# Performance work log

Measured on AMD Instinct MI355X. Metric: run time of the kernel, lower is better.

The kernel has to match this reference:

```python
import jax, jax.numpy as jnp
import numpy as np

N, E, D, H, O = 100000, 1600000, 256, 128, 64


def setup_inputs() -> dict:
    key = jax.random.key(0)
    ks = jax.random.split(key, 10)
    x = jax.random.normal(ks[0], (N, D), dtype=jnp.float32)
    # edges without self loops (original adds remaining self loops itself)
    row = jax.random.randint(ks[1], (E,), 0, N)
    off = jax.random.randint(ks[2], (E,), 1, N)
    col = (row + off) % N
    edge_index = jnp.stack([row, col]).astype(jnp.int64)
    # positive PPMI edge weights (stand-in for cached random-walk PPMI values)
    ppmi_edge_weight = jax.random.uniform(ks[3], (E,), dtype=jnp.float32, minval=0.1, maxval=1.0)
    # glorot-style weights (shared between GCN and PPMI branches, as in the module)
    W1 = jax.random.normal(ks[4], (D, H), dtype=jnp.float32) * np.sqrt(2.0 / (D + H))
    b1 = jnp.zeros((H,), dtype=jnp.float32)
    W2 = jax.random.normal(ks[5], (H, O), dtype=jnp.float32) * np.sqrt(2.0 / (H + O))
    b2 = jnp.zeros((O,), dtype=jnp.float32)
    dense_w = jax.random.normal(ks[6], (O, 1), dtype=jnp.float32) * np.sqrt(2.0 / (O + 1))
    dense_b = jnp.zeros((1,), dtype=jnp.float32)
    return {"x": x, "edge_index": edge_index, "ppmi_edge_weight": ppmi_edge_weight,
            "W1": W1, "b1": b1, "W2": W2, "b2": b2,
            "dense_w": dense_w, "dense_b": dense_b}


def _sym_norm(row, col, ew, n):
    # deg^-0.5[row] * w * deg^-0.5[col], deg from scatter-add over source index
    deg = jax.ops.segment_sum(ew, row, num_segments=n)
    dis = jnp.where(deg > 0, deg ** -0.5, 0.0)
    return dis[row] * ew * dis[col]


def _gconv(h, W, b, row, col, norm, n):
    hw = h @ W                              # [N, F_out]
    msg = norm[:, None] * hw[row]           # gather + scale, [E', F_out]
    return jax.ops.segment_sum(msg, col, num_segments=n) + b


def reference(x, edge_index, ppmi_edge_weight, W1, b1, W2, b2, dense_w, dense_b):
    n = x.shape[0]
    row = edge_index[0].astype(jnp.int32)
    col = edge_index[1].astype(jnp.int32)
    sl = jnp.arange(n, dtype=jnp.int32)
    row_sl = jnp.concatenate([row, sl])
    col_sl = jnp.concatenate([col, sl])
    ones_sl = jnp.ones((n,), dtype=x.dtype)

    # GCN branch: edge_weight = 1, plus self loops (fill_value = 1)
    gcn_ew = jnp.concatenate([jnp.ones((row.shape[0],), dtype=x.dtype), ones_sl])
    gnorm = _sym_norm(row_sl, col_sl, gcn_ew, n)
    g = jax.nn.relu(_gconv(x, W1, b1, row_sl, col_sl, gnorm, n))  # dropout p in eval -> identity
    g = _gconv(g, W2, b2, row_sl, col_sl, gnorm, n)

    # PPMI branch: precomputed positive weights, plus self loops
    ppmi_ew = jnp.concatenate([ppmi_edge_weight.astype(x.dtype), ones_sl])
    pnorm = _sym_norm(row_sl, col_sl, ppmi_ew, n)
    p = jax.nn.relu(_gconv(x, W1, b1, row_sl, col_sl, pnorm, n))
    p = _gconv(p, W2, b2, row_sl, col_sl, pnorm, n)

    stacked = jnp.stack([g, p], axis=1)                 # [N, 2, O]
    logits = stacked @ dense_w + dense_b                # [N, 2, 1]
    w = jax.nn.softmax(logits, axis=1)
    return jnp.sum(stacked * w, axis=1)                 # [N, O]
```

## Files before the change

kernel.cpp:

```cpp
#include <hip/hip_runtime.h>
#include <hip/hip_bf16.h>
#include <math.h>

#define DD 256
#define HH 128
#define OO 64

#define EPB 8192
#define BKT 512

typedef __attribute__((ext_vector_type(8))) __bf16 bf16x8;
typedef __attribute__((ext_vector_type(4))) __bf16 bf16x4;
typedef __attribute__((ext_vector_type(4))) float f32x4;

__device__ inline float2 bf2_to_f2(unsigned u) {
    float2 r;
    r.x = __uint_as_float(u << 16);
    r.y = __uint_as_float(u & 0xffff0000u);
    return r;
}

__global__ void part_count_kernel(const int* __restrict__ row, const int* __restrict__ col,
                                  int e, int nb,
                                  int* __restrict__ cnt_col, int* __restrict__ cnt_row) {
    __shared__ int hc[256], hr[256];
    int t = threadIdx.x;
    hc[t] = 0; hr[t] = 0;
    __syncthreads();
    int base = blockIdx.x * EPB;
    int lim  = min(EPB, e - base);
    for (int i = t; i < lim; i += 256) {
        atomicAdd(&hc[col[base + i] >> 9], 1);
        atomicAdd(&hr[row[base + i] >> 9], 1);
    }
    __syncthreads();
    if (t < nb) {
        cnt_col[blockIdx.x * nb + t] = hc[t];
        cnt_row[blockIdx.x * nb + t] = hr[t];
    }
}

__global__ void scan_blocks_kernel(const int* __restrict__ cnt_col, const int* __restrict__ cnt_row,
                                   int* __restrict__ base_col, int* __restrict__ base_row,
                                   int* __restrict__ tot_col, int* __restrict__ tot_row,
                                   int nblk, int nb) {
    __shared__ int s[256];
    int side = (blockIdx.x >= (unsigned)nb) ? 1 : 0;
    int b = blockIdx.x - side * nb;
    const int* cnt = side ? cnt_row : cnt_col;
    int* base = side ? base_row : base_col;
    int* tot  = side ? tot_row  : tot_col;
    int t = threadIdx.x;
    int v = (t < nblk) ? cnt[(size_t)t * nb + b] : 0;
    s[t] = v;
    __syncthreads();
    for (int off = 1; off < 256; off <<= 1) {
        int u = (t >= off) ? s[t - off] : 0;
        __syncthreads();
        s[t] += u;
        __syncthreads();
    }
    if (t < nblk) base[(size_t)t * nb + b] = s[t] - v;
    if (t == 255) tot[b] = s[255];
}

__global__ void scan_tots_kernel(const int* __restrict__ tot_col, const int* __restrict__ tot_row,
                                 int* __restrict__ bb_col, int* __restrict__ bb_row, int nb) {
    __shared__ int s[256];
    int t = threadIdx.x;
    int v = (t < nb) ? tot_col[t] : 0;
    s[t] = v;
    __syncthreads();
    for (int off = 1; off < 256; off <<= 1) {
        int u = (t >= off) ? s[t - off] : 0;
        __syncthreads();
        s[t] += u;
        __syncthreads();
    }
    if (t < nb) bb_col[t] = s[t] - v;
    __syncthreads();
    int v2 = (t < nb) ? tot_row[t] : 0;
    s[t] = v2;
    __syncthreads();
    for (int off = 1; off < 256; off <<= 1) {
        int u = (t >= off) ? s[t - off] : 0;
        __syncthreads();
        s[t] += u;
        __syncthreads();
    }
    if (t < nb) bb_row[t] = s[t] - v2;
}

__global__ void add_bases_kernel(int* __restrict__ base_col, int* __restrict__ base_row,
                                 const int* __restrict__ bb_col, const int* __restrict__ bb_row,
                                 int* __restrict__ row_ptr, int n, int e, int nblk, int nb) {
    int side = (blockIdx.x >= (unsigned)nb) ? 1 : 0;
    int b = blockIdx.x - side * nb;
    int* base = side ? base_row : base_col;
    int add   = side ? bb_row[b] : bb_col[b];
    for (int t = threadIdx.x; t < nblk; t += blockDim.x) base[(size_t)t * nb + b] += add;
    if (blockIdx.x == 0 && threadIdx.x == 0) row_ptr[n] = e;
}

__global__ void part_scatter_kernel(const int* __restrict__ row, const int* __restrict__ col,
                                    const float* __restrict__ ppmi,
                                    const int* __restrict__ base_col, const int* __restrict__ base_row,
                                    int4* __restrict__ tmp_col, int2* __restrict__ tmp_row,
                                    int e, int nb) {
    __shared__ int cc[256], cr[256];
    int t = threadIdx.x;
    if (t < nb) {
        cc[t] = base_col[blockIdx.x * nb + t];
        cr[t] = base_row[blockIdx.x * nb + t];
    }
    __syncthreads();
    int base = blockIdx.x * EPB;
    int lim  = min(EPB, e - base);
    for (int i = t; i < lim; i += 256) {
        int r = row[base + i], c = col[base + i];
        int w = __float_as_int(ppmi[base + i]);
        int sc = atomicAdd(&cc[c >> 9], 1);
        tmp_col[sc] = make_int4(c, r, w, 0);
        int sr = atomicAdd(&cr[r >> 9], 1);
        tmp_row[sr] = make_int2(r, w);
    }
}

__global__ void deg_bucket_kernel(const int2* __restrict__ tmp_row,
                                  const int* __restrict__ bb_row, const int* __restrict__ tot_row,
                                  float* __restrict__ dis_g, float* __restrict__ dis_p, int n) {
    __shared__ float dg[BKT], dp[BKT];
    int t = threadIdx.x;
    for (int j = t; j < BKT; j += 256) { dg[j] = 1.0f; dp[j] = 1.0f; }
    __syncthreads();
    int b = blockIdx.x;
    int beg = bb_row[b], cnt = tot_row[b];
    for (int i = t; i < cnt; i += 256) {
        int2 cell = tmp_row[beg + i];
        int lr = cell.x & (BKT - 1);
        atomicAdd(&dg[lr], 1.0f);
        atomicAdd(&dp[lr], __int_as_float(cell.y));
    }
    __syncthreads();
    int rb = b << 9;
    for (int j = t; j < BKT; j += 256) {
        int g = rb + j;
        if (g < n) {
            dis_g[g] = rsqrtf(dg[j]);
            dis_p[g] = rsqrtf(dp[j]);
        }
    }
}

__launch_bounds__(512)
__global__ void csr_bucket_kernel(const int4* __restrict__ tmp_col,
                                  const int* __restrict__ bb_col, const int* __restrict__ tot_col,
                                  const float* __restrict__ dis_g, const float* __restrict__ dis_p,
                                  int* __restrict__ row_ptr, int* __restrict__ csr_src,
                                  float* __restrict__ csr_wg, float* __restrict__ csr_wp, int n) {
    __shared__ int hist[BKT], s[BKT], cur[BKT];
    int t = threadIdx.x;
    hist[t] = 0;
    __syncthreads();
    int b = blockIdx.x;
    int beg = bb_col[b], cnt = tot_col[b];
    for (int i = t; i < cnt; i += BKT) atomicAdd(&hist[tmp_col[beg + i].x & (BKT - 1)], 1);
    __syncthreads();
    int own = hist[t];
    s[t] = own;
    __syncthreads();
    for (int off = 1; off < BKT; off <<= 1) {
        int v = (t >= off) ? s[t - off] : 0;
        __syncthreads();
        s[t] += v;
        __syncthreads();
    }
    int gslot = beg + s[t] - own;
    cur[t] = gslot;
    int gc = (b << 9) + t;
    if (gc < n) row_ptr[gc] = gslot;
    __syncthreads();
    for (int i = t; i < cnt; i += BKT) {
        int4 cell = tmp_col[beg + i];
        int lc = cell.x & (BKT - 1);
        int slot = atomicAdd(&cur[lc], 1);
        int r = cell.y;
        float w = __int_as_float(cell.z);
        csr_src[slot] = r;
        csr_wg[slot]  = dis_g[r];
        csr_wp[slot]  = dis_p[r] * w;
    }
}

__global__ void conv_w_kernel(const float* __restrict__ W, __bf16* __restrict__ Bh,
                              __bf16* __restrict__ Bl, int K, int N) {
    int i = blockIdx.x * blockDim.x + threadIdx.x;
    if (i >= K * N) return;
    int k = i / N, nn = i % N;
    float v = W[i];
    __bf16 h = (__bf16)v;
    Bh[(size_t)nn * K + k] = h;
    Bl[(size_t)nn * K + k] = (__bf16)(v - (float)h);
}

template<int BM, int BN, typename OT>
__launch_bounds__(256, 2)
__global__ void mfma_gemm_kernel(const float* __restrict__ A,
                                 const __bf16* __restrict__ Bth, const __bf16* __restrict__ Btl,
                                 OT* __restrict__ C, int M, int K) {
    constexpr int BK  = 32;
    constexpr int LDK = BK + 8;
    constexpr int WM  = BM / 4;
    constexpr int MT  = WM / 16;
    constexpr int NT  = BN / 16;
    __shared__ __bf16 Ash[BM * LDK];
    __shared__ __bf16 Asl[BM * LDK];
    __shared__ __bf16 Bsh[BN * LDK];
    __shared__ __bf16 Bsl[BN * LDK];

    const int tid  = threadIdx.x;
    const int wave = tid >> 6;
    const int lane = tid & 63;
    const int quad = lane >> 4;
    const int l16  = lane & 15;
    const int row0 = blockIdx.x * BM;

    f32x4 acc[MT][NT] = {};

    for (int k0 = 0; k0 < K; k0 += BK) {
#pragma unroll
        for (int p = 0; p < BM / 32; ++p) {
            int lin = p * 256 + tid;
            int r   = lin >> 3;
            int kc  = (lin & 7) * 4;
            int gr  = row0 + r;
            float4 v;
            if (gr < M) v = *(const float4*)(A + (size_t)gr * K + k0 + kc);
            else        v = make_float4(0.f, 0.f, 0.f, 0.f);
            __bf16 h0 = (__bf16)v.x, h1 = (__bf16)v.y, h2 = (__bf16)v.z, h3 = (__bf16)v.w;
            __bf16 l0 = (__bf16)(v.x - (float)h0), l1 = (__bf16)(v.y - (float)h1);
            __bf16 l2 = (__bf16)(v.z - (float)h2), l3 = (__bf16)(v.w - (float)h3);
            *(bf16x4*)&Ash[r * LDK + kc] = (bf16x4){h0, h1, h2, h3};
            *(bf16x4*)&Asl[r * LDK + kc] = (bf16x4){l0, l1, l2, l3};
        }
#pragma unroll
        for (int p = 0; p < BN / 64; ++p) {
            int lin = p * 256 + tid;
            int r   = lin >> 2;
            int kc  = (lin & 3) * 8;
            *(uint4*)&Bsh[r * LDK + kc] = *(const uint4*)(Bth + (size_t)r * K + k0 + kc);
            *(uint4*)&Bsl[r * LDK + kc] = *(const uint4*)(Btl + (size_t)r * K + k0 + kc);
        }
        __syncthreads();

        bf16x8 bh[NT], bl[NT];
#pragma unroll
        for (int j = 0; j < NT; ++j) {
            bh[j] = *(const bf16x8*)&Bsh[(j * 16 + l16) * LDK + quad * 8];
            bl[j] = *(const bf16x8*)&Bsl[(j * 16 + l16) * LDK + quad * 8];
        }
#pragma unroll
        for (int i = 0; i < MT; ++i) {
            int m = wave * WM + i * 16 + l16;
            bf16x8 ah = *(const bf16x8*)&Ash[m * LDK + quad * 8];
            bf16x8 al = *(const bf16x8*)&Asl[m * LDK + quad * 8];
#pragma unroll
            for (int j = 0; j < NT; ++j) {
                acc[i][j] = __builtin_amdgcn_mfma_f32_16x16x32_bf16(ah, bh[j], acc[i][j], 0, 0, 0);
                acc[i][j] = __builtin_amdgcn_mfma_f32_16x16x32_bf16(ah, bl[j], acc[i][j], 0, 0, 0);
                acc[i][j] = __builtin_amdgcn_mfma_f32_16x16x32_bf16(al, bh[j], acc[i][j], 0, 0, 0);
            }
        }
        __syncthreads();
    }

#pragma unroll
    for (int i = 0; i < MT; ++i) {
#pragma unroll
        for (int rg = 0; rg < 4; ++rg) {
            int gr = row0 + wave * WM + i * 16 + quad * 4 + rg;
            if (gr < M) {
#pragma unroll
                for (int j = 0; j < NT; ++j)
                    C[(size_t)gr * BN + j * 16 + l16] = (OT)acc[i][j][rg];
            }
        }
    }
}

__global__ void agg1_pull_kernel(const int* __restrict__ row_ptr, const int* __restrict__ csr_src,
                                 const float* __restrict__ csr_wg, const float* __restrict__ csr_wp,
                                 const __bf16* __restrict__ hw1,
                                 const float* __restrict__ dis_g, const float* __restrict__ dis_p,
                                 const float* __restrict__ b1,
                                 float* __restrict__ g_out, float* __restrict__ p_out, int n) {
    int c    = blockIdx.x * 4 + (threadIdx.x >> 6);
    int lane = threadIdx.x & 63;
    if (c >= n) return;
    int beg = row_ptr[c], end = row_ptr[c + 1];
    int f2 = lane * 2;
    float sgx = 0.f, sgy = 0.f, spx = 0.f, spy = 0.f;
    int t = beg;
    for (; t + 2 <= end; t += 2) {
        int r0 = csr_src[t], r1 = csr_src[t + 1];
        float wg0 = csr_wg[t], wg1 = csr_wg[t + 1];
        float wp0 = csr_wp[t], wp1 = csr_wp[t + 1];
        float2 h0 = bf2_to_f2(*(const unsigned*)(hw1 + (size_t)r0 * HH + f2));
        float2 h1 = bf2_to_f2(*(const unsigned*)(hw1 + (size_t)r1 * HH + f2));
        sgx += wg0 * h0.x + wg1 * h1.x;
        sgy += wg0 * h0.y + wg1 * h1.y;
        spx += wp0 * h0.x + wp1 * h1.x;
        spy += wp0 * h0.y + wp1 * h1.y;
    }
    if (t < end) {
        int r0 = csr_src[t];
        float wg0 = csr_wg[t], wp0 = csr_wp[t];
        float2 h0 = bf2_to_f2(*(const unsigned*)(hw1 + (size_t)r0 * HH + f2));
        sgx += wg0 * h0.x; sgy += wg0 * h0.y;
        spx += wp0 * h0.x; spy += wp0 * h0.y;
    }
    float dgc = dis_g[c], dpc = dis_p[c];
    size_t idx = (size_t)c * HH + f2;
    float2 hs = bf2_to_f2(*(const unsigned*)(hw1 + idx));
    float bx = b1[f2], by = b1[f2 + 1];
    float gx = dgc * sgx + dgc * dgc * hs.x + bx;
    float gy = dgc * sgy + dgc * dgc * hs.y + by;
    float px = dpc * spx + dpc * dpc * hs.x + bx;
    float py = dpc * spy + dpc * dpc * hs.y + by;
    float2 go, po;
    go.x = gx > 0.f ? gx : 0.f;  go.y = gy > 0.f ? gy : 0.f;
    po.x = px > 0.f ? px : 0.f;  po.y = py > 0.f ? py : 0.f;
    *(float2*)&g_out[idx] = go;
    *(float2*)&p_out[idx] = po;
}

__global__ void agg2_final_kernel(const int* __restrict__ row_ptr, const int* __restrict__ csr_src,
                                  const float* __restrict__ csr_wg, const float* __restrict__ csr_wp,
                                  const __bf16* __restrict__ hw2_g, const __bf16* __restrict__ hw2_p,
                                  const float* __restrict__ dis_g, const float* __restrict__ dis_p,
                                  const float* __restrict__ b2,
                                  const float* __restrict__ dense_w, const float* __restrict__ dense_b,
                                  float* __restrict__ out, int n) {
    int c = blockIdx.x * 4 + (threadIdx.x >> 6);
    int f = threadIdx.x & 63;
    if (c >= n) return;
    int beg = row_ptr[c], end = row_ptr[c + 1];
    float sg = 0.f, sp = 0.f;
    int t = beg;
    for (; t + 2 <= end; t += 2) {
        int r0 = csr_src[t], r1 = csr_src[t + 1];
        float wg0 = csr_wg[t], wg1 = csr_wg[t + 1];
        float wp0 = csr_wp[t], wp1 = csr_wp[t + 1];
        float hg0 = (float)hw2_g[(size_t)r0 * OO + f], hg1 = (float)hw2_g[(size_t)r1 * OO + f];
        float hp0 = (float)hw2_p[(size_t)r0 * OO + f], hp1 = (float)hw2_p[(size_t)r1 * OO + f];
        sg += wg0 * hg0 + wg1 * hg1;
        sp += wp0 * hp0 + wp1 * hp1;
    }
    if (t < end) {
        int r0 = csr_src[t];
        sg += csr_wg[t] * (float)hw2_g[(size_t)r0 * OO + f];
        sp += csr_wp[t] * (float)hw2_p[(size_t)r0 * OO + f];
    }
    float dgc = dis_g[c], dpc = dis_p[c];
    size_t idx = (size_t)c * OO + f;
    float bb = b2[f];
    float gv = dgc * sg + dgc * dgc * (float)hw2_g[idx] + bb;
    float pv = dpc * sp + dpc * dpc * (float)hw2_p[idx] + bb;
    float dw = dense_w[f];
    float lg = gv * dw, lp = pv * dw;
#pragma unroll
    for (int off = 32; off > 0; off >>= 1) {
        lg += __shfl_xor(lg, off, 64);
        lp += __shfl_xor(lp, off, 64);
    }
    lg += dense_b[0];
    lp += dense_b[0];
    float m  = fmaxf(lg, lp);
    float eg = expf(lg - m), ep = expf(lp - m);
    float wgt = eg / (eg + ep);
    out[idx] = wgt * gv + (1.0f - wgt) * pv;
}

extern "C" void kernel_launch(void* const* d_in, const int* in_sizes, int n_in,
                              void* d_out, int out_size, void* d_ws, size_t ws_size,
                              hipStream_t stream) {
    const float* x    = (const float*)d_in[0];
    const int*   ei   = (const int*)d_in[1];
    const float* ppmi = (const float*)d_in[2];
    const float* W1   = (const float*)d_in[3];
    const float* b1   = (const float*)d_in[4];
    const float* W2   = (const float*)d_in[5];
    const float* b2   = (const float*)d_in[6];
    const float* dw   = (const float*)d_in[7];
    const float* db   = (const float*)d_in[8];
    float* out = (float*)d_out;

    const int n = in_sizes[0] / DD;
    const int e = in_sizes[2];
    const int* row = ei;
    const int* col = ei + e;

    const int nb   = (n + BKT - 1) / BKT;
    const int nblk = (e + EPB - 1) / EPB;

    float* ws     = (float*)d_ws;
    float* dis_g  = ws;
    float* dis_p  = dis_g + n;
    __bf16* hw1   = (__bf16*)(dis_p + n);
    float* g1     = (float*)(hw1 + (size_t)n * HH);
    float* p1     = g1  + (size_t)n * HH;
    float* csr_wg = p1  + (size_t)n * HH;
    float* csr_wp = csr_wg + e;
    __bf16* bt1h  = (__bf16*)(csr_wp + e);
    __bf16* bt1l  = bt1h + (size_t)DD * HH;
    __bf16* bt2h  = bt1l + (size_t)DD * HH;
    __bf16* bt2l  = bt2h + (size_t)HH * OO;
    int* row_ptr  = (int*)(bt2l + (size_t)HH * OO);
    int* csr_src  = row_ptr + (n + 1);
    int* cnt_col  = csr_src + e;
    int* base_col = cnt_col + (size_t)nblk * nb;
    int* cnt_row  = base_col + (size_t)nblk * nb;
    int* base_row = cnt_row + (size_t)nblk * nb;
    int* bb_col   = base_row + (size_t)nblk * nb;
    int* tot_col  = bb_col + nb;
    int* bb_row   = tot_col + nb;
    int* tot_row  = bb_row + nb;
    int4* tmp_col = (int4*)g1;
    int2* tmp_row = (int2*)p1;
    __bf16* hw2   = hw1;
    __bf16* hw2_g = hw2;
    __bf16* hw2_p = hw2 + (size_t)n * OO;

    const int T = 256;

    part_count_kernel<<<nblk, T, 0, stream>>>(row, col, e, nb, cnt_col, cnt_row);
    scan_blocks_kernel<<<2 * nb, T, 0, stream>>>(cnt_col, cnt_row, base_col, base_row,
                                                 tot_col, tot_row, nblk, nb);
    scan_tots_kernel<<<1, T, 0, stream>>>(tot_col, tot_row, bb_col, bb_row, nb);
    add_bases_kernel<<<2 * nb, T, 0, stream>>>(base_col, base_row, bb_col, bb_row,
                                               row_ptr, n, e, nblk, nb);
    part_scatter_kernel<<<nblk, T, 0, stream>>>(row, col, ppmi, base_col, base_row,
                                                tmp_col, tmp_row, e, nb);
    deg_bucket_kernel<<<nb, T, 0, stream>>>(tmp_row, bb_row, tot_row, dis_g, dis_p, n);
    csr_bucket_kernel<<<nb, BKT, 0, stream>>>(tmp_col, bb_col, tot_col, dis_g, dis_p,
                                              row_ptr, csr_src, csr_wg, csr_wp, n);

    conv_w_kernel<<<(DD * HH + T - 1) / T, T, 0, stream>>>(W1, bt1h, bt1l, DD, HH);
    conv_w_kernel<<<(HH * OO + T - 1) / T, T, 0, stream>>>(W2, bt2h, bt2l, HH, OO);

    mfma_gemm_kernel<128, HH, __bf16><<<(n + 127) / 128, 256, 0, stream>>>(x, bt1h, bt1l, hw1, n, DD);
    agg1_pull_kernel<<<(n + 3) / 4, 256, 0, stream>>>(row_ptr, csr_src, csr_wg, csr_wp,
                                                      hw1, dis_g, dis_p, b1, g1, p1, n);
    mfma_gemm_kernel<128, OO, __bf16><<<(2 * n + 127) / 128, 256, 0, stream>>>(g1, bt2h, bt2l, hw2, 2 * n, HH);
    agg2_final_kernel<<<(n + 3) / 4, 256, 0, stream>>>(row_ptr, csr_src, csr_wg, csr_wp,
                                                       hw2_g, hw2_p, dis_g, dis_p, b2, dw, db, out, n);
}
```

Measured before the change: 624.1 us.

## Pack CSR metadata into int4, interleave layer-2 g/p features, unroll gathers by four

Merges the CSR source index and both per-edge weights into one 16-byte int4 record, and packs the two degree-normalisation arrays into a single float2 array. The second GEMM now writes the GCN and PPMI outputs interleaved per feature, so agg2 fetches both with one 4-byte gather per neighbour instead of two separate 2-byte gathers from different rows. Both aggregation kernels unroll the neighbour loop to four to put more loads in flight. The cost is a padded 16-byte meta record (4 bytes unused) and strided, scattered 2-byte stores in the GEMM epilogue.

```diff
diff --git a/kernel.cpp b/kernel.cpp
--- a/kernel.cpp
+++ b/kernel.cpp
@@ -128,7 +128,7 @@
 
 __global__ void deg_bucket_kernel(const int2* __restrict__ tmp_row,
                                   const int* __restrict__ bb_row, const int* __restrict__ tot_row,
-                                  float* __restrict__ dis_g, float* __restrict__ dis_p, int n) {
+                                  float2* __restrict__ dis, int n) {
     __shared__ float dg[BKT], dp[BKT];
     int t = threadIdx.x;
     for (int j = t; j < BKT; j += 256) { dg[j] = 1.0f; dp[j] = 1.0f; }
@@ -145,19 +145,15 @@
     int rb = b << 9;
     for (int j = t; j < BKT; j += 256) {
         int g = rb + j;
-        if (g < n) {
-            dis_g[g] = rsqrtf(dg[j]);
-            dis_p[g] = rsqrtf(dp[j]);
-        }
+        if (g < n) dis[g] = make_float2(rsqrtf(dg[j]), rsqrtf(dp[j]));
     }
 }
 
 __launch_bounds__(512)
 __global__ void csr_bucket_kernel(const int4* __restrict__ tmp_col,
                                   const int* __restrict__ bb_col, const int* __restrict__ tot_col,
-                                  const float* __restrict__ dis_g, const float* __restrict__ dis_p,
-                                  int* __restrict__ row_ptr, int* __restrict__ csr_src,
-                                  float* __restrict__ csr_wg, float* __restrict__ csr_wp, int n) {
+                                  const float2* __restrict__ dis,
+                                  int* __restrict__ row_ptr, int4* __restrict__ csr_meta, int n) {
     __shared__ int hist[BKT], s[BKT], cur[BKT];
     int t = threadIdx.x;
     hist[t] = 0;
@@ -186,9 +182,8 @@
         int slot = atomicAdd(&cur[lc], 1);
         int r = cell.y;
         float w = __int_as_float(cell.z);
-        csr_src[slot] = r;
-        csr_wg[slot]  = dis_g[r];
-        csr_wp[slot]  = dis_p[r] * w;
+        float2 d = dis[r];
+        csr_meta[slot] = make_int4(r, __float_as_int(d.x), __float_as_int(d.y * w), 0);
     }
 }
 
@@ -203,11 +198,11 @@
     Bl[(size_t)nn * K + k] = (__bf16)(v - (float)h);
 }
 
-template<int BM, int BN, typename OT>
+template<int BM, int BN, typename OT, bool ILV>
 __launch_bounds__(256, 2)
 __global__ void mfma_gemm_kernel(const float* __restrict__ A,
                                  const __bf16* __restrict__ Bth, const __bf16* __restrict__ Btl,
-                                 OT* __restrict__ C, int M, int K) {
+                                 OT* __restrict__ C, int M, int K, int nHalf) {
     constexpr int BK  = 32;
     constexpr int LDK = BK + 8;
     constexpr int WM  = BM / 4;
@@ -280,18 +275,25 @@
         for (int rg = 0; rg < 4; ++rg) {
             int gr = row0 + wave * WM + i * 16 + quad * 4 + rg;
             if (gr < M) {
-#pragma unroll
-                for (int j = 0; j < NT; ++j)
-                    C[(size_t)gr * BN + j * 16 + l16] = (OT)acc[i][j][rg];
+                if constexpr (ILV) {
+                    int s = (gr >= nHalf) ? 1 : 0;
+                    size_t base = (size_t)(gr - s * nHalf) * (BN * 2) + s;
+#pragma unroll
+                    for (int j = 0; j < NT; ++j)
+                        C[base + (size_t)(j * 16 + l16) * 2] = (OT)acc[i][j][rg];
+                } else {
+#pragma unroll
+                    for (int j = 0; j < NT; ++j)
+                        C[(size_t)gr * BN + j * 16 + l16] = (OT)acc[i][j][rg];
+                }
             }
         }
     }
 }
 
-__global__ void agg1_pull_kernel(const int* __restrict__ row_ptr, const int* __restrict__ csr_src,
-                                 const float* __restrict__ csr_wg, const float* __restrict__ csr_wp,
+__global__ void agg1_pull_kernel(const int* __restrict__ row_ptr, const int4* __restrict__ meta,
                                  const __bf16* __restrict__ hw1,
-                                 const float* __restrict__ dis_g, const float* __restrict__ dis_p,
+                                 const float2* __restrict__ dis,
                                  const float* __restrict__ b1,
                                  float* __restrict__ g_out, float* __restrict__ p_out, int n) {
     int c    = blockIdx.x * 4 + (threadIdx.x >> 6);
@@ -301,32 +303,38 @@
     int f2 = lane * 2;
     float sgx = 0.f, sgy = 0.f, spx = 0.f, spy = 0.f;
     int t = beg;
-    for (; t + 2 <= end; t += 2) {
-        int r0 = csr_src[t], r1 = csr_src[t + 1];
-        float wg0 = csr_wg[t], wg1 = csr_wg[t + 1];
-        float wp0 = csr_wp[t], wp1 = csr_wp[t + 1];
-        float2 h0 = bf2_to_f2(*(const unsigned*)(hw1 + (size_t)r0 * HH + f2));
-        float2 h1 = bf2_to_f2(*(const unsigned*)(hw1 + (size_t)r1 * HH + f2));
-        sgx += wg0 * h0.x + wg1 * h1.x;
-        sgy += wg0 * h0.y + wg1 * h1.y;
-        spx += wp0 * h0.x + wp1 * h1.x;
-        spy += wp0 * h0.y + wp1 * h1.y;
-    }
-    if (t < end) {
-        int r0 = csr_src[t];
-        float wg0 = csr_wg[t], wp0 = csr_wp[t];
-        float2 h0 = bf2_to_f2(*(const unsigned*)(hw1 + (size_t)r0 * HH + f2));
+    for (; t + 4 <= end; t += 4) {
+        int4 m0 = meta[t], m1 = meta[t + 1], m2 = meta[t + 2], m3 = meta[t + 3];
+        unsigned u0 = *(const unsigned*)(hw1 + ((size_t)m0.x << 7) + f2);
+        unsigned u1 = *(const unsigned*)(hw1 + ((size_t)m1.x << 7) + f2);
+        unsigned u2 = *(const unsigned*)(hw1 + ((size_t)m2.x << 7) + f2);
+        unsigned u3 = *(const unsigned*)(hw1 + ((size_t)m3.x << 7) + f2);
+        float2 h0 = bf2_to_f2(u0), h1 = bf2_to_f2(u1);
+        float2 h2 = bf2_to_f2(u2), h3 = bf2_to_f2(u3);
+        float wg0 = __int_as_float(m0.y), wp0 = __int_as_float(m0.z);
+        float wg1 = __int_as_float(m1.y), wp1 = __int_as_float(m1.z);
+        float wg2 = __int_as_float(m2.y), wp2 = __int_as_float(m2.z);
+        float wg3 = __int_as_float(m3.y), wp3 = __int_as_float(m3.z);
+        sgx += wg0 * h0.x + wg1 * h1.x + wg2 * h2.x + wg3 * h3.x;
+        sgy += wg0 * h0.y + wg1 * h1.y + wg2 * h2.y + wg3 * h3.y;
+        spx += wp0 * h0.x + wp1 * h1.x + wp2 * h2.x + wp3 * h3.x;
+        spy += wp0 * h0.y + wp1 * h1.y + wp2 * h2.y + wp3 * h3.y;
+    }
+    for (; t < end; ++t) {
+        int4 m0 = meta[t];
+        float2 h0 = bf2_to_f2(*(const unsigned*)(hw1 + ((size_t)m0.x << 7) + f2));
+        float wg0 = __int_as_float(m0.y), wp0 = __int_as_float(m0.z);
         sgx += wg0 * h0.x; sgy += wg0 * h0.y;
         spx += wp0 * h0.x; spy += wp0 * h0.y;
     }
-    float dgc = dis_g[c], dpc = dis_p[c];
-    size_t idx = (size_t)c * HH + f2;
+    float2 d = dis[c];
+    size_t idx = ((size_t)c << 7) + f2;
     float2 hs = bf2_to_f2(*(const unsigned*)(hw1 + idx));
-    float bx = b1[f2], by = b1[f2 + 1];
-    float gx = dgc * sgx + dgc * dgc * hs.x + bx;
-    float gy = dgc * sgy + dgc * dgc * hs.y + by;
-    float px = dpc * spx + dpc * dpc * hs.x + bx;
-    float py = dpc * spy + dpc * dpc * hs.y + by;
+    float2 bv = *(const float2*)(b1 + f2);
+    float gx = d.x * sgx + d.x * d.x * hs.x + bv.x;
+    float gy = d.x * sgy + d.x * d.x * hs.y + bv.y;
+    float px = d.y * spx + d.y * d.y * hs.x + bv.x;
+    float py = d.y * spy + d.y * d.y * hs.y + bv.y;
     float2 go, po;
     go.x = gx > 0.f ? gx : 0.f;  go.y = gy > 0.f ? gy : 0.f;
     po.x = px > 0.f ? px : 0.f;  po.y = py > 0.f ? py : 0.f;
@@ -334,10 +342,9 @@
     *(float2*)&p_out[idx] = po;
 }
 
-__global__ void agg2_final_kernel(const int* __restrict__ row_ptr, const int* __restrict__ csr_src,
-                                  const float* __restrict__ csr_wg, const float* __restrict__ csr_wp,
-                                  const __bf16* __restrict__ hw2_g, const __bf16* __restrict__ hw2_p,
-                                  const float* __restrict__ dis_g, const float* __restrict__ dis_p,
+__global__ void agg2_final_kernel(const int* __restrict__ row_ptr, const int4* __restrict__ meta,
+                                  const __bf16* __restrict__ hw2i,
+                                  const float2* __restrict__ dis,
                                   const float* __restrict__ b2,
                                   const float* __restrict__ dense_w, const float* __restrict__ dense_b,
                                   float* __restrict__ out, int n) {
@@ -345,29 +352,35 @@
     int f = threadIdx.x & 63;
     if (c >= n) return;
     int beg = row_ptr[c], end = row_ptr[c + 1];
+    int f2 = f * 2;
     float sg = 0.f, sp = 0.f;
     int t = beg;
-    for (; t + 2 <= end; t += 2) {
-        int r0 = csr_src[t], r1 = csr_src[t + 1];
-        float wg0 = csr_wg[t], wg1 = csr_wg[t + 1];
-        float wp0 = csr_wp[t], wp1 = csr_wp[t + 1];
-        float hg0 = (float)hw2_g[(size_t)r0 * OO + f], hg1 = (float)hw2_g[(size_t)r1 * OO + f];
-        float hp0 = (float)hw2_p[(size_t)r0 * OO + f], hp1 = (float)hw2_p[(size_t)r1 * OO + f];
-        sg += wg0 * hg0 + wg1 * hg1;
-        sp += wp0 * hp0 + wp1 * hp1;
-    }
-    if (t < end) {
-        int r0 = csr_src[t];
-        sg += csr_wg[t] * (float)hw2_g[(size_t)r0 * OO + f];
-        sp += csr_wp[t] * (float)hw2_p[(size_t)r0 * OO + f];
-    }
-    float dgc = dis_g[c], dpc = dis_p[c];
-    size_t idx = (size_t)c * OO + f;
+    for (; t + 4 <= end; t += 4) {
+        int4 m0 = meta[t], m1 = meta[t + 1], m2 = meta[t + 2], m3 = meta[t + 3];
+        unsigned u0 = *(const unsigned*)(hw2i + ((size_t)m0.x << 7) + f2);
+        unsigned u1 = *(const unsigned*)(hw2i + ((size_t)m1.x << 7) + f2);
+        unsigned u2 = *(const unsigned*)(hw2i + ((size_t)m2.x << 7) + f2);
+        unsigned u3 = *(const unsigned*)(hw2i + ((size_t)m3.x << 7) + f2);
+        float2 g0 = bf2_to_f2(u0), g1v = bf2_to_f2(u1);
+        float2 g2 = bf2_to_f2(u2), g3v = bf2_to_f2(u3);
+        sg += __int_as_float(m0.y) * g0.x + __int_as_float(m1.y) * g1v.x
+            + __int_as_float(m2.y) * g2.x + __int_as_float(m3.y) * g3v.x;
+        sp += __int_as_float(m0.z) * g0.y + __int_as_float(m1.z) * g1v.y
+            + __int_as_float(m2.z) * g2.y + __int_as_float(m3.z) * g3v.y;
+    }
+    for (; t < end; ++t) {
+        int4 m0 = meta[t];
+        float2 g0 = bf2_to_f2(*(const unsigned*)(hw2i + ((size_t)m0.x << 7) + f2));
+        sg += __int_as_float(m0.y) * g0.x;
+        sp += __int_as_float(m0.z) * g0.y;
+    }
+    float2 d = dis[c];
+    float2 gps = bf2_to_f2(*(const unsigned*)(hw2i + ((size_t)c << 7) + f2));
     float bb = b2[f];
-    float gv = dgc * sg + dgc * dgc * (float)hw2_g[idx] + bb;
-    float pv = dpc * sp + dpc * dpc * (float)hw2_p[idx] + bb;
-    float dw = dense_w[f];
-    float lg = gv * dw, lp = pv * dw;
+    float gv = d.x * sg + d.x * d.x * gps.x + bb;
+    float pv = d.y * sp + d.y * d.y * gps.y + bb;
+    float dwv = dense_w[f];
+    float lg = gv * dwv, lp = pv * dwv;
 #pragma unroll
     for (int off = 32; off > 0; off >>= 1) {
         lg += __shfl_xor(lg, off, 64);
@@ -378,7 +391,7 @@
     float m  = fmaxf(lg, lp);
     float eg = expf(lg - m), ep = expf(lp - m);
     float wgt = eg / (eg + ep);
-    out[idx] = wgt * gv + (1.0f - wgt) * pv;
+    out[(size_t)c * OO + f] = wgt * gv + (1.0f - wgt) * pv;
 }
 
 extern "C" void kernel_launch(void* const* d_in, const int* in_sizes, int n_in,
@@ -403,33 +416,28 @@
     const int nb   = (n + BKT - 1) / BKT;
     const int nblk = (e + EPB - 1) / EPB;
 
-    float* ws     = (float*)d_ws;
-    float* dis_g  = ws;
-    float* dis_p  = dis_g + n;
-    __bf16* hw1   = (__bf16*)(dis_p + n);
-    float* g1     = (float*)(hw1 + (size_t)n * HH);
-    float* p1     = g1  + (size_t)n * HH;
-    float* csr_wg = p1  + (size_t)n * HH;
-    float* csr_wp = csr_wg + e;
-    __bf16* bt1h  = (__bf16*)(csr_wp + e);
-    __bf16* bt1l  = bt1h + (size_t)DD * HH;
-    __bf16* bt2h  = bt1l + (size_t)DD * HH;
-    __bf16* bt2l  = bt2h + (size_t)HH * OO;
-    int* row_ptr  = (int*)(bt2l + (size_t)HH * OO);
-    int* csr_src  = row_ptr + (n + 1);
-    int* cnt_col  = csr_src + e;
-    int* base_col = cnt_col + (size_t)nblk * nb;
-    int* cnt_row  = base_col + (size_t)nblk * nb;
-    int* base_row = cnt_row + (size_t)nblk * nb;
-    int* bb_col   = base_row + (size_t)nblk * nb;
-    int* tot_col  = bb_col + nb;
-    int* bb_row   = tot_col + nb;
-    int* tot_row  = bb_row + nb;
-    int4* tmp_col = (int4*)g1;
-    int2* tmp_row = (int2*)p1;
-    __bf16* hw2   = hw1;
-    __bf16* hw2_g = hw2;
-    __bf16* hw2_p = hw2 + (size_t)n * OO;
+    float* ws      = (float*)d_ws;
+    float2* dis    = (float2*)ws;
+    __bf16* hw1    = (__bf16*)(ws + 2 * (size_t)n);
+    float* g1      = (float*)(hw1 + (size_t)n * HH);
+    float* p1      = g1 + (size_t)n * HH;
+    int4* csr_meta = (int4*)(p1 + (size_t)n * HH);
+    __bf16* bt1h   = (__bf16*)(csr_meta + e);
+    __bf16* bt1l   = bt1h + (size_t)DD * HH;
+    __bf16* bt2h   = bt1l + (size_t)DD * HH;
+    __bf16* bt2l   = bt2h + (size_t)HH * OO;
+    int* row_ptr   = (int*)(bt2l + (size_t)HH * OO);
+    int* cnt_col   = row_ptr + (n + 1);
+    int* base_col  = cnt_col + (size_t)nblk * nb;
+    int* cnt_row   = base_col + (size_t)nblk * nb;
+    int* base_row  = cnt_row + (size_t)nblk * nb;
+    int* bb_col    = base_row + (size_t)nblk * nb;
+    int* tot_col   = bb_col + nb;
+    int* bb_row    = tot_col + nb;
+    int* tot_row   = bb_row + nb;
+    int4* tmp_col  = (int4*)g1;
+    int2* tmp_row  = (int2*)p1;
+    __bf16* hw2i   = hw1;
 
     const int T = 256;
 
@@ -441,17 +449,18 @@
                                                row_ptr, n, e, nblk, nb);
     part_scatter_kernel<<<nblk, T, 0, stream>>>(row, col, ppmi, base_col, base_row,
                                                 tmp_col, tmp_row, e, nb);
-    deg_bucket_kernel<<<nb, T, 0, stream>>>(tmp_row, bb_row, tot_row, dis_g, dis_p, n);
-    csr_bucket_kernel<<<nb, BKT, 0, stream>>>(tmp_col, bb_col, tot_col, dis_g, dis_p,
-                                              row_ptr, csr_src, csr_wg, csr_wp, n);
+    deg_bucket_kernel<<<nb, T, 0, stream>>>(tmp_row, bb_row, tot_row, dis, n);
+    csr_bucket_kernel<<<nb, BKT, 0, stream>>>(tmp_col, bb_col, tot_col, dis,
+                                              row_ptr, csr_meta, n);
 
     conv_w_kernel<<<(DD * HH + T - 1) / T, T, 0, stream>>>(W1, bt1h, bt1l, DD, HH);
     conv_w_kernel<<<(HH * OO + T - 1) / T, T, 0, stream>>>(W2, bt2h, bt2l, HH, OO);
 
-    mfma_gemm_kernel<128, HH, __bf16><<<(n + 127) / 128, 256, 0, stream>>>(x, bt1h, bt1l, hw1, n, DD);
-    agg1_pull_kernel<<<(n + 3) / 4, 256, 0, stream>>>(row_ptr, csr_src, csr_wg, csr_wp,
-                                                      hw1, dis_g, dis_p, b1, g1, p1, n);
-    mfma_gemm_kernel<128, OO, __bf16><<<(2 * n + 127) / 128, 256, 0, stream>>>(g1, bt2h, bt2l, hw2, 2 * n, HH);
-    agg2_final_kernel<<<(n + 3) / 4, 256, 0, stream>>>(row_ptr, csr_src, csr_wg, csr_wp,
-                                                       hw2_g, hw2_p, dis_g, dis_p, b2, dw, db, out, n);
-}
+    mfma_gemm_kernel<128, HH, __bf16, false><<<(n + 127) / 128, 256, 0, stream>>>(
+        x, bt1h, bt1l, hw1, n, DD, 0);
+    agg1_pull_kernel<<<(n + 3) / 4, 256, 0, stream>>>(row_ptr, csr_meta, hw1, dis, b1, g1, p1, n);
+    mfma_gemm_kernel<128, OO, __bf16, true><<<(2 * n + 127) / 128, 256, 0, stream>>>(
+        g1, bt2h, bt2l, hw2i, 2 * n, HH, n);
+    agg2_final_kernel<<<(n + 3) / 4, 256, 0, stream>>>(row_ptr, csr_meta, hw2i, dis,
+                                                       b2, dw, db, out, n);
+}
```

Result: faster. 554.7 us (-11.1%).
